# Kernel tuning notes

Measured on AMD Instinct MI355X. Metric: run time of the kernel, lower is better.

Reference implementation:

```python
import jax, jax.numpy as jnp
import numpy as np

B, S, E, H = 4, 2048, 1024, 16
DK = E // H  # 64


def setup_inputs() -> dict:
    key = jax.random.key(0)
    ks = jax.random.split(key, 11)
    s_in = 1.0 / np.sqrt(E)
    return {
        "query": jax.random.normal(ks[0], (B, S, E), jnp.float32),
        "key_": jax.random.normal(ks[1], (B, S, E), jnp.float32),
        "value": jax.random.normal(ks[2], (B, S, E), jnp.float32),
        # nn.Linear weights stored as [out, in]; applied as x @ W.T + b
        "Wq": jax.random.uniform(ks[3], (E, E), jnp.float32, -s_in, s_in),
        "bq": jax.random.uniform(ks[4], (E,), jnp.float32, -s_in, s_in),
        "Wk": jax.random.uniform(ks[5], (E, E), jnp.float32, -s_in, s_in),
        "bk": jax.random.uniform(ks[6], (E,), jnp.float32, -s_in, s_in),
        "Wv": jax.random.uniform(ks[7], (E, E), jnp.float32, -s_in, s_in),
        "bv": jax.random.uniform(ks[8], (E,), jnp.float32, -s_in, s_in),
        "Wo": jax.random.uniform(ks[9], (E, E), jnp.float32, -s_in, s_in),
        "bo": jax.random.uniform(ks[10], (E,), jnp.float32, -s_in, s_in),
    }


def reference(query, key_, value, Wq, bq, Wk, bk, Wv, bv, Wo, bo):
    scale = 1.0 / np.sqrt(DK).astype(np.float32)
    Q = query @ Wq.T + bq   # [B,S,E]
    K = key_ @ Wk.T + bk
    V = value @ Wv.T + bv
    # split heads: [B,S,H,DK] (slicing dim -1 into contiguous per-head chunks)
    Qh = Q.reshape(B, S, H, DK)
    Kh = K.reshape(B, S, H, DK)
    Vh = V.reshape(B, S, H, DK)
    scores = jnp.einsum('bqhd,bkhd->bhqk', Qh, Kh) * scale  # [B,H,S,S]
    probs = jax.nn.softmax(scores, axis=-1)
    ctx = jnp.einsum('bhqk,bkhd->bqhd', probs, Vh).reshape(B, S, E)
    out = ctx @ Wo.T + bo
    return out
```

## Files before the change

kernel.cpp:

```cpp
#include <hip/hip_runtime.h>
#include <stdint.h>
#include <stddef.h>

constexpr int BB = 4, SS = 2048, EE = 1024, HH = 16, DKH = 64;
constexpr int MM = BB * SS;
constexpr float SM_SCALE_LOG2 = 0.18033688011112042f;

typedef unsigned short u16;
typedef __attribute__((ext_vector_type(8))) short bf16x8;
typedef __attribute__((ext_vector_type(8))) unsigned short u16x8;
typedef __attribute__((ext_vector_type(4))) float f32x4;
typedef __attribute__((ext_vector_type(16))) float f32x16;
typedef __attribute__((ext_vector_type(2))) unsigned int u32x2;
typedef __attribute__((ext_vector_type(4))) unsigned int u32x4;

__device__ __forceinline__ u16 f2bf(float f) {
  unsigned u = __builtin_bit_cast(unsigned, f);
  u += 0x7FFFu + ((u >> 16) & 1u);
  return (u16)(u >> 16);
}

__device__ __forceinline__ unsigned pack2(float lo, float hi) {
  unsigned r;
  asm("v_cvt_pk_bf16_f32 %0, %1, %2" : "=v"(r) : "v"(lo), "v"(hi));
  return r;
}

__device__ __forceinline__ void gld16(const void* g, void* l) {
  __builtin_amdgcn_global_load_lds(
      (const __attribute__((address_space(1))) unsigned int*)g,
      (__attribute__((address_space(3))) unsigned int*)l, 16, 0, 0);
}

struct Cvt3 { const float* in[3]; u16* out[3]; };
struct Cvt4 { const float* in[4]; u16* out[4]; };

__global__ void cvt_bf16_x3(Cvt3 p, int n8) {
  int i = blockIdx.x * 256 + threadIdx.x;
  if (i >= n8) return;
  const int z = blockIdx.y;
  const float4* src = (const float4*)p.in[z] + (size_t)i * 2;
  float4 a = src[0], b = src[1];
  u16x8 v;
  v[0] = f2bf(a.x); v[1] = f2bf(a.y); v[2] = f2bf(a.z); v[3] = f2bf(a.w);
  v[4] = f2bf(b.x); v[5] = f2bf(b.y); v[6] = f2bf(b.z); v[7] = f2bf(b.w);
  *((u16x8*)p.out[z] + i) = v;
}

__global__ void cvt_bf16_x4(Cvt4 p, int n8) {
  int i = blockIdx.x * 256 + threadIdx.x;
  if (i >= n8) return;
  const int z = blockIdx.y;
  const float4* src = (const float4*)p.in[z] + (size_t)i * 2;
  float4 a = src[0], b = src[1];
  u16x8 v;
  v[0] = f2bf(a.x); v[1] = f2bf(a.y); v[2] = f2bf(a.z); v[3] = f2bf(a.w);
  v[4] = f2bf(b.x); v[5] = f2bf(b.y); v[6] = f2bf(b.z); v[7] = f2bf(b.w);
  *((u16x8*)p.out[z] + i) = v;
}

struct GemmPtrs {
  const u16* A[3];
  const u16* W[3];
  const float* bias[3];
  void* C[3];
  float scale[3];
  int mode[3];
};

__global__ __launch_bounds__(256, 4) void gemm32(GemmPtrs p, int M, int N, int K) {
  __shared__ __align__(16) u16 SA[2][64 * 64];
  __shared__ __align__(16) u16 SB[2][64 * 64];
  const int t = threadIdx.x, l = t & 63, w = t >> 6;
  const int lq = l & 31, hi = l >> 5;
  const int wm = w >> 1, wn = w & 1;
  const int z = blockIdx.z;
  const u16* A = p.A[z];
  const u16* W = p.W[z];
  const float* bias = p.bias[z];

  const int nwg = gridDim.x * gridDim.y;
  const int o = blockIdx.y * gridDim.x + blockIdx.x;
  const int sw = (o & 7) * (nwg >> 3) + (o >> 3);
  const int n0 = (sw % gridDim.x) * 128;
  const int m0 = (sw / gridDim.x) * 128;

  f32x16 acc[2][2];
#pragma unroll
  for (int i = 0; i < 2; ++i)
#pragma unroll
    for (int j = 0; j < 2; ++j)
#pragma unroll
      for (int r = 0; r < 16; ++r) acc[i][j][r] = 0.f;

  auto stage = [&](int buf, int kt) {
#pragma unroll
    for (int i = 0; i < 2; ++i) {
      const int ci = i * 256 + t;
      const int r = ci >> 3, P = ci & 7;
      const int L = P ^ (r & 7);
      const int m = r + ((L & 4) << 4);
      const int kc = L & 3;
      const int dst = (i * 256 + (t & ~63)) * 16;
      gld16(A + (size_t)(m0 + m) * K + kt * 32 + kc * 8, (char*)&SA[buf][0] + dst);
      gld16(W + (size_t)(n0 + m) * K + kt * 32 + kc * 8, (char*)&SB[buf][0] + dst);
    }
  };

  stage(0, 0);
  __syncthreads();
  int cur = 0;
  const int NT = K >> 5;
  const int lsw = lq & 7;
  for (int kt = 0; kt < NT; ++kt) {
    if (kt + 1 < NT) stage(cur ^ 1, kt + 1);
    const u16* Ac = &SA[cur][0];
    const u16* Bc = &SB[cur][0];
    __builtin_amdgcn_s_setprio(1);
#pragma unroll
    for (int ks = 0; ks < 2; ++ks) {
      const int ca = ((wm << 2) + (ks << 1) + hi) ^ lsw;
      const int cb = ((wn << 2) + (ks << 1) + hi) ^ lsw;
      bf16x8 a0 = *(const bf16x8*)(Ac + lq * 64 + ca * 8);
      bf16x8 a1 = *(const bf16x8*)(Ac + (32 + lq) * 64 + ca * 8);
      bf16x8 b0 = *(const bf16x8*)(Bc + lq * 64 + cb * 8);
      bf16x8 b1 = *(const bf16x8*)(Bc + (32 + lq) * 64 + cb * 8);
      acc[0][0] = __builtin_amdgcn_mfma_f32_32x32x16_bf16(a0, b0, acc[0][0], 0, 0, 0);
      acc[0][1] = __builtin_amdgcn_mfma_f32_32x32x16_bf16(a0, b1, acc[0][1], 0, 0, 0);
      acc[1][0] = __builtin_amdgcn_mfma_f32_32x32x16_bf16(a1, b0, acc[1][0], 0, 0, 0);
      acc[1][1] = __builtin_amdgcn_mfma_f32_32x32x16_bf16(a1, b1, acc[1][1], 0, 0, 0);
    }
    __builtin_amdgcn_s_setprio(0);
    __syncthreads();
    cur ^= 1;
  }

  const float sc = p.scale[z];
  const int mode = p.mode[z];
#pragma unroll
  for (int fr = 0; fr < 2; ++fr) {
#pragma unroll
    for (int fc = 0; fc < 2; ++fc) {
      const int col = n0 + wn * 64 + fc * 32 + lq;
      const float bv = bias[col];
#pragma unroll
      for (int g = 0; g < 4; ++g) {
        const int mb = m0 + wm * 64 + fr * 32 + 8 * g + 4 * hi;
        float v[4];
#pragma unroll
        for (int j = 0; j < 4; ++j) v[j] = (acc[fr][fc][4 * g + j] + bv) * sc;
        if (mode == 1) {
#pragma unroll
          for (int j = 0; j < 4; ++j)
            ((float*)p.C[z])[(size_t)(mb + j) * N + col] = v[j];
        } else if (mode == 0) {
#pragma unroll
          for (int j = 0; j < 4; ++j)
            ((u16*)p.C[z])[(size_t)(mb + j) * N + col] = f2bf(v[j]);
        } else {
          const int b = mb >> 11, s = mb & 2047;
          u16* dst = (u16*)p.C[z] +
                     ((size_t)((b * 16 + (col >> 6)) * 64 + (col & 63))) * SS + s;
          uint2 pk;
          pk.x = pack2(v[0], v[1]);
          pk.y = pack2(v[2], v[3]);
          *(uint2*)dst = pk;
        }
      }
    }
  }
}

__global__ __launch_bounds__(256, 4) void attn_fwd3(const u16* __restrict__ Q,
                                                    const u16* __restrict__ K,
                                                    const u16* __restrict__ Vt,
                                                    u16* __restrict__ C) {
  __shared__ __align__(16) u16 Ks[2][64 * 64];
  __shared__ __align__(16) u16 Vs[2][64 * 64];

  const int t = threadIdx.x, l = t & 63, w = t >> 6;
  const int lq = l & 31, hi = l >> 5;
  const int q0 = blockIdx.x * 128;
  const int bh = blockIdx.y, bb = bh >> 4, hh = bh & 15;

  const u16* qp = Q + ((size_t)(bb * SS + q0 + w * 32 + lq)) * EE + hh * 64 + hi * 8;
  bf16x8 qf[4];
  qf[0] = *(const bf16x8*)(qp);
  qf[1] = *(const bf16x8*)(qp + 16);
  qf[2] = *(const bf16x8*)(qp + 32);
  qf[3] = *(const bf16x8*)(qp + 48);

  const u16* Kbase = K + (size_t)bb * SS * EE + hh * 64;
  const u16* Vbase = Vt + (size_t)bh * DKH * SS;

  f32x16 accA, accB;
  f32x16 z16;
#pragma unroll
  for (int i = 0; i < 16; ++i) { accA[i] = 0.f; accB[i] = 0.f; z16[i] = 0.f; }
  float lsum = 0.0f;

  auto stage = [&](int buf, int kt) {
#pragma unroll
    for (int i = 0; i < 2; ++i) {
      const int slot = i * 256 + t;
      const int row = slot >> 3, pc = slot & 7;
      const int lc = pc ^ (row & 7);
      const int lbyte = (i * 256 + (t & ~63)) * 16;
      gld16(Kbase + (size_t)(kt * 64 + row) * EE + lc * 8, (char*)&Ks[buf][0] + lbyte);
      gld16(Vbase + (size_t)row * SS + kt * 64 + lc * 8, (char*)&Vs[buf][0] + lbyte);
    }
  };

  auto mkfrag = [&](const f32x16& p, int base) -> bf16x8 {
    unsigned A0 = pack2(p[base + 0], p[base + 1]);
    unsigned A1 = pack2(p[base + 2], p[base + 3]);
    unsigned B0 = pack2(p[base + 4], p[base + 5]);
    unsigned B1 = pack2(p[base + 6], p[base + 7]);
    u32x2 r0 = __builtin_amdgcn_permlane32_swap(A0, B0, false, false);
    u32x2 r1 = __builtin_amdgcn_permlane32_swap(A1, B1, false, false);
    u32x4 fr;
    fr[0] = r0[0]; fr[1] = r1[0]; fr[2] = r0[1]; fr[3] = r1[1];
    return __builtin_bit_cast(bf16x8, fr);
  };

  stage(0, 0);
  __syncthreads();
  int cur = 0;
  for (int kt = 0; kt < SS / 64; ++kt) {
    if (kt + 1 < SS / 64) stage(cur ^ 1, kt + 1);
    const u16* Kc = &Ks[cur][0];
    const u16* Vc = &Vs[cur][0];

    f32x16 s0, s1;
    __builtin_amdgcn_s_setprio(1);
    {
      const int c = hi ^ (lq & 7);
      bf16x8 kf0 = *(const bf16x8*)(Kc + lq * 64 + c * 8);
      bf16x8 kf1 = *(const bf16x8*)(Kc + (32 + lq) * 64 + c * 8);
      s0 = __builtin_amdgcn_mfma_f32_32x32x16_bf16(kf0, qf[0], z16, 0, 0, 0);
      s1 = __builtin_amdgcn_mfma_f32_32x32x16_bf16(kf1, qf[0], z16, 0, 0, 0);
    }
#pragma unroll
    for (int m = 1; m < 4; ++m) {
      const int c = (2 * m + hi) ^ (lq & 7);
      bf16x8 kf0 = *(const bf16x8*)(Kc + lq * 64 + c * 8);
      bf16x8 kf1 = *(const bf16x8*)(Kc + (32 + lq) * 64 + c * 8);
      s0 = __builtin_amdgcn_mfma_f32_32x32x16_bf16(kf0, qf[m], s0, 0, 0, 0);
      s1 = __builtin_amdgcn_mfma_f32_32x32x16_bf16(kf1, qf[m], s1, 0, 0, 0);
    }
    __builtin_amdgcn_s_setprio(0);

#pragma unroll
    for (int i = 0; i < 16; ++i) {
      s0[i] = __builtin_amdgcn_exp2f(s0[i]);
      s1[i] = __builtin_amdgcn_exp2f(s1[i]);
    }
    float sa = 0.f, sb = 0.f, sc2 = 0.f, sd = 0.f;
#pragma unroll
    for (int i = 0; i < 8; ++i) {
      sa += s0[i]; sb += s0[i + 8];
      sc2 += s1[i]; sd += s1[i + 8];
    }
    lsum += (sa + sb) + (sc2 + sd);

    bf16x8 pf[4];
    pf[0] = mkfrag(s0, 0);
    pf[1] = mkfrag(s0, 8);
    pf[2] = mkfrag(s1, 0);
    pf[3] = mkfrag(s1, 8);

    __builtin_amdgcn_s_setprio(1);
#pragma unroll
    for (int s = 0; s < 4; ++s) {
      const int c = (2 * s + hi) ^ (lq & 7);
      bf16x8 vf0 = *(const bf16x8*)(Vc + lq * 64 + c * 8);
      bf16x8 vf1 = *(const bf16x8*)(Vc + (32 + lq) * 64 + c * 8);
      accA = __builtin_amdgcn_mfma_f32_32x32x16_bf16(vf0, pf[s], accA, 0, 0, 0);
      accB = __builtin_amdgcn_mfma_f32_32x32x16_bf16(vf1, pf[s], accB, 0, 0, 0);
    }
    __builtin_amdgcn_s_setprio(0);
    __syncthreads();
    cur ^= 1;
  }

  const float inv = 1.0f / (lsum + __shfl_xor(lsum, 32));
  char* Tw = (char*)&Ks[0][0] + w * 4096;
#pragma unroll
  for (int g = 0; g < 4; ++g) {
    uint2 pa, pb;
    pa.x = pack2(accA[4 * g + 0] * inv, accA[4 * g + 1] * inv);
    pa.y = pack2(accA[4 * g + 2] * inv, accA[4 * g + 3] * inv);
    pb.x = pack2(accB[4 * g + 0] * inv, accB[4 * g + 1] * inv);
    pb.y = pack2(accB[4 * g + 2] * inv, accB[4 * g + 3] * inv);
    const int sub = 8 * hi, sw = (lq & 7) << 4;
    *(uint2*)(Tw + lq * 128 + (((g) << 4) ^ sw) + sub) = pa;
    *(uint2*)(Tw + lq * 128 + (((4 + g) << 4) ^ sw) + sub) = pb;
  }
  const int qr0 = l >> 3, ch = l & 7;
#pragma unroll
  for (int ps = 0; ps < 4; ++ps) {
    const int qr = ps * 8 + qr0;
    u32x4 vv = *(const u32x4*)(Tw + qr * 128 + ((ch ^ (qr & 7)) << 4));
    u16* dst = C + ((size_t)(bb * SS + q0 + w * 32 + qr)) * EE + hh * 64 + ch * 8;
    *(u32x4*)dst = vv;
  }
}

extern "C" void kernel_launch(void* const* d_in, const int* in_sizes, int n_in,
                              void* d_out, int out_size, void* d_ws, size_t ws_size,
                              hipStream_t stream) {
  (void)in_sizes; (void)n_in; (void)out_size; (void)ws_size;
  const float* query = (const float*)d_in[0];
  const float* key_  = (const float*)d_in[1];
  const float* value = (const float*)d_in[2];
  const float* Wq = (const float*)d_in[3];
  const float* bq = (const float*)d_in[4];
  const float* Wk = (const float*)d_in[5];
  const float* bk = (const float*)d_in[6];
  const float* Wv = (const float*)d_in[7];
  const float* bv = (const float*)d_in[8];
  const float* Wo = (const float*)d_in[9];
  const float* bo = (const float*)d_in[10];

  char* ws = (char*)d_ws;
  const size_t SZX = (size_t)MM * EE * 2;
  const size_t SZW = (size_t)EE * EE * 2;
  u16* Xq  = (u16*)(ws + 0 * SZX);
  u16* Xk  = (u16*)(ws + 1 * SZX);
  u16* Xv  = (u16*)(ws + 2 * SZX);
  u16* Qb  = (u16*)(ws + 3 * SZX);
  u16* Kb  = (u16*)(ws + 4 * SZX);
  u16* Vtb = (u16*)(ws + 5 * SZX);
  u16* Cb  = (u16*)(ws + 6 * SZX);
  u16* Wqb = (u16*)(ws + 7 * SZX + 0 * SZW);
  u16* Wkb = (u16*)(ws + 7 * SZX + 1 * SZW);
  u16* Wvb = (u16*)(ws + 7 * SZX + 2 * SZW);
  u16* Wob = (u16*)(ws + 7 * SZX + 3 * SZW);

  const int n8x = MM * EE / 8;
  const int n8w = EE * EE / 8;

  Cvt3 cx{};
  cx.in[0] = query; cx.in[1] = key_; cx.in[2] = value;
  cx.out[0] = Xq; cx.out[1] = Xk; cx.out[2] = Xv;
  cvt_bf16_x3<<<dim3(n8x / 256, 3), 256, 0, stream>>>(cx, n8x);

  Cvt4 cw{};
  cw.in[0] = Wq; cw.in[1] = Wk; cw.in[2] = Wv; cw.in[3] = Wo;
  cw.out[0] = Wqb; cw.out[1] = Wkb; cw.out[2] = Wvb; cw.out[3] = Wob;
  cvt_bf16_x4<<<dim3(n8w / 256, 4), 256, 0, stream>>>(cw, n8w);

  GemmPtrs g{};
  g.A[0] = Xq; g.A[1] = Xk; g.A[2] = Xv;
  g.W[0] = Wqb; g.W[1] = Wkb; g.W[2] = Wvb;
  g.bias[0] = bq; g.bias[1] = bk; g.bias[2] = bv;
  g.C[0] = Qb; g.C[1] = Kb; g.C[2] = Vtb;
  g.scale[0] = SM_SCALE_LOG2; g.scale[1] = 1.0f; g.scale[2] = 1.0f;
  g.mode[0] = 0; g.mode[1] = 0; g.mode[2] = 2;
  gemm32<<<dim3(EE / 128, MM / 128, 3), 256, 0, stream>>>(g, MM, EE, EE);

  attn_fwd3<<<dim3(SS / 128, BB * HH), 256, 0, stream>>>(Qb, Kb, Vtb, Cb);

  GemmPtrs g2{};
  g2.A[0] = Cb; g2.W[0] = Wob; g2.bias[0] = bo; g2.C[0] = d_out;
  g2.scale[0] = 1.0f; g2.mode[0] = 1;
  gemm32<<<dim3(EE / 128, MM / 128, 1), 256, 0, stream>>>(g2, MM, EE, EE);
}
```

Baseline: 211.8 us.

## Fuse fp32-to-bf16 activation conversion into QKV projection GEMM A-tile staging

New measurement: 217.4 us. 2.7% more time.

```diff
diff --git a/kernel.cpp b/kernel.cpp
--- a/kernel.cpp
+++ b/kernel.cpp
@@ -32,20 +32,7 @@
       (__attribute__((address_space(3))) unsigned int*)l, 16, 0, 0);
 }
 
-struct Cvt3 { const float* in[3]; u16* out[3]; };
 struct Cvt4 { const float* in[4]; u16* out[4]; };
-
-__global__ void cvt_bf16_x3(Cvt3 p, int n8) {
-  int i = blockIdx.x * 256 + threadIdx.x;
-  if (i >= n8) return;
-  const int z = blockIdx.y;
-  const float4* src = (const float4*)p.in[z] + (size_t)i * 2;
-  float4 a = src[0], b = src[1];
-  u16x8 v;
-  v[0] = f2bf(a.x); v[1] = f2bf(a.y); v[2] = f2bf(a.z); v[3] = f2bf(a.w);
-  v[4] = f2bf(b.x); v[5] = f2bf(b.y); v[6] = f2bf(b.z); v[7] = f2bf(b.w);
-  *((u16x8*)p.out[z] + i) = v;
-}
 
 __global__ void cvt_bf16_x4(Cvt4 p, int n8) {
   int i = blockIdx.x * 256 + threadIdx.x;
@@ -61,6 +48,7 @@
 
 struct GemmPtrs {
   const u16* A[3];
+  const float* A32[3];
   const u16* W[3];
   const float* bias[3];
   void* C[3];
@@ -68,6 +56,7 @@
   int mode[3];
 };
 
+template <int AF32>
 __global__ __launch_bounds__(256, 4) void gemm32(GemmPtrs p, int M, int N, int K) {
   __shared__ __align__(16) u16 SA[2][64 * 64];
   __shared__ __align__(16) u16 SB[2][64 * 64];
@@ -76,6 +65,7 @@
   const int wm = w >> 1, wn = w & 1;
   const int z = blockIdx.z;
   const u16* A = p.A[z];
+  const float* Af = p.A32[z];
   const u16* W = p.W[z];
   const float* bias = p.bias[z];
 
@@ -93,27 +83,76 @@
 #pragma unroll
       for (int r = 0; r < 16; ++r) acc[i][j][r] = 0.f;
 
-  auto stage = [&](int buf, int kt) {
+  auto stageB = [&](int buf, int kt) {
 #pragma unroll
     for (int i = 0; i < 2; ++i) {
       const int ci = i * 256 + t;
       const int r = ci >> 3, P = ci & 7;
       const int L = P ^ (r & 7);
-      const int m = r + ((L & 4) << 4);
+      const int mr = r + ((L & 4) << 4);
       const int kc = L & 3;
-      const int dst = (i * 256 + (t & ~63)) * 16;
-      gld16(A + (size_t)(m0 + m) * K + kt * 32 + kc * 8, (char*)&SA[buf][0] + dst);
-      gld16(W + (size_t)(n0 + m) * K + kt * 32 + kc * 8, (char*)&SB[buf][0] + dst);
-    }
-  };
-
-  stage(0, 0);
+      gld16(W + (size_t)(n0 + mr) * K + kt * 32 + kc * 8,
+            (char*)&SB[buf][0] + (i * 256 + (t & ~63)) * 16);
+    }
+  };
+  auto stageAb = [&](int buf, int kt) {
+#pragma unroll
+    for (int i = 0; i < 2; ++i) {
+      const int ci = i * 256 + t;
+      const int r = ci >> 3, P = ci & 7;
+      const int L = P ^ (r & 7);
+      const int mr = r + ((L & 4) << 4);
+      const int kc = L & 3;
+      gld16(A + (size_t)(m0 + mr) * K + kt * 32 + kc * 8,
+            (char*)&SA[buf][0] + (i * 256 + (t & ~63)) * 16);
+    }
+  };
+  float4 av[2][2];
+  auto loadAf = [&](int kt) {
+#pragma unroll
+    for (int i = 0; i < 2; ++i) {
+      const int u = i * 256 + t;
+      const int mr = u >> 2, kc = u & 3;
+      const float4* src = (const float4*)(Af + (size_t)(m0 + mr) * K + kt * 32 + kc * 8);
+      av[i][0] = src[0];
+      av[i][1] = src[1];
+    }
+  };
+  auto writeAf = [&](int buf) {
+#pragma unroll
+    for (int i = 0; i < 2; ++i) {
+      const int u = i * 256 + t;
+      const int mr = u >> 2, kc = u & 3;
+      const int r = mr & 63;
+      const int P = (((mr >> 6) << 2) + kc) ^ (r & 7);
+      u32x4 pk;
+      pk[0] = pack2(av[i][0].x, av[i][0].y);
+      pk[1] = pack2(av[i][0].z, av[i][0].w);
+      pk[2] = pack2(av[i][1].x, av[i][1].y);
+      pk[3] = pack2(av[i][1].z, av[i][1].w);
+      *(u32x4*)((char*)&SA[buf][0] + r * 128 + P * 16) = pk;
+    }
+  };
+
+  if (AF32) {
+    loadAf(0);
+    writeAf(0);
+  } else {
+    stageAb(0, 0);
+  }
+  stageB(0, 0);
   __syncthreads();
+
   int cur = 0;
   const int NT = K >> 5;
   const int lsw = lq & 7;
   for (int kt = 0; kt < NT; ++kt) {
-    if (kt + 1 < NT) stage(cur ^ 1, kt + 1);
+    const bool nx = (kt + 1 < NT);
+    if (nx) {
+      if (AF32) loadAf(kt + 1);
+      else stageAb(cur ^ 1, kt + 1);
+      stageB(cur ^ 1, kt + 1);
+    }
     const u16* Ac = &SA[cur][0];
     const u16* Bc = &SB[cur][0];
     __builtin_amdgcn_s_setprio(1);
@@ -131,6 +170,10 @@
       acc[1][1] = __builtin_amdgcn_mfma_f32_32x32x16_bf16(a1, b1, acc[1][1], 0, 0, 0);
     }
     __builtin_amdgcn_s_setprio(0);
+    if (AF32 && nx) {
+      __builtin_amdgcn_sched_barrier(0);
+      writeAf(cur ^ 1);
+    }
     __syncthreads();
     cur ^= 1;
   }
@@ -325,25 +368,16 @@
   char* ws = (char*)d_ws;
   const size_t SZX = (size_t)MM * EE * 2;
   const size_t SZW = (size_t)EE * EE * 2;
-  u16* Xq  = (u16*)(ws + 0 * SZX);
-  u16* Xk  = (u16*)(ws + 1 * SZX);
-  u16* Xv  = (u16*)(ws + 2 * SZX);
-  u16* Qb  = (u16*)(ws + 3 * SZX);
-  u16* Kb  = (u16*)(ws + 4 * SZX);
-  u16* Vtb = (u16*)(ws + 5 * SZX);
-  u16* Cb  = (u16*)(ws + 6 * SZX);
-  u16* Wqb = (u16*)(ws + 7 * SZX + 0 * SZW);
-  u16* Wkb = (u16*)(ws + 7 * SZX + 1 * SZW);
-  u16* Wvb = (u16*)(ws + 7 * SZX + 2 * SZW);
-  u16* Wob = (u16*)(ws + 7 * SZX + 3 * SZW);
-
-  const int n8x = MM * EE / 8;
+  u16* Qb  = (u16*)(ws + 0 * SZX);
+  u16* Kb  = (u16*)(ws + 1 * SZX);
+  u16* Vtb = (u16*)(ws + 2 * SZX);
+  u16* Cb  = (u16*)(ws + 3 * SZX);
+  u16* Wqb = (u16*)(ws + 4 * SZX + 0 * SZW);
+  u16* Wkb = (u16*)(ws + 4 * SZX + 1 * SZW);
+  u16* Wvb = (u16*)(ws + 4 * SZX + 2 * SZW);
+  u16* Wob = (u16*)(ws + 4 * SZX + 3 * SZW);
+
   const int n8w = EE * EE / 8;
-
-  Cvt3 cx{};
-  cx.in[0] = query; cx.in[1] = key_; cx.in[2] = value;
-  cx.out[0] = Xq; cx.out[1] = Xk; cx.out[2] = Xv;
-  cvt_bf16_x3<<<dim3(n8x / 256, 3), 256, 0, stream>>>(cx, n8x);
 
   Cvt4 cw{};
   cw.in[0] = Wq; cw.in[1] = Wk; cw.in[2] = Wv; cw.in[3] = Wo;
@@ -351,18 +385,18 @@
   cvt_bf16_x4<<<dim3(n8w / 256, 4), 256, 0, stream>>>(cw, n8w);
 
   GemmPtrs g{};
-  g.A[0] = Xq; g.A[1] = Xk; g.A[2] = Xv;
+  g.A32[0] = query; g.A32[1] = key_; g.A32[2] = value;
   g.W[0] = Wqb; g.W[1] = Wkb; g.W[2] = Wvb;
   g.bias[0] = bq; g.bias[1] = bk; g.bias[2] = bv;
   g.C[0] = Qb; g.C[1] = Kb; g.C[2] = Vtb;
   g.scale[0] = SM_SCALE_LOG2; g.scale[1] = 1.0f; g.scale[2] = 1.0f;
   g.mode[0] = 0; g.mode[1] = 0; g.mode[2] = 2;
-  gemm32<<<dim3(EE / 128, MM / 128, 3), 256, 0, stream>>>(g, MM, EE, EE);
+  gemm32<1><<<dim3(EE / 128, MM / 128, 3), 256, 0, stream>>>(g, MM, EE, EE);
 
   attn_fwd3<<<dim3(SS / 128, BB * HH), 256, 0, stream>>>(Qb, Kb, Vtb, Cb);
 
   GemmPtrs g2{};
   g2.A[0] = Cb; g2.W[0] = Wob; g2.bias[0] = bo; g2.C[0] = d_out;
   g2.scale[0] = 1.0f; g2.mode[0] = 1;
-  gemm32<<<dim3(EE / 128, MM / 128, 1), 256, 0, stream>>>(g2, MM, EE, EE);
-}
+  gemm32<0><<<dim3(EE / 128, MM / 128, 1), 256, 0, stream>>>(g2, MM, EE, EE);
+}
```

## Triple-buffer GEMM LDS stages with manual vmcnt waits and single barrier

Applied to the files above, without the earlier changes.

Result: slower. 217.2 us (+2.6%).

```diff
diff --git a/kernel.cpp b/kernel.cpp
--- a/kernel.cpp
+++ b/kernel.cpp
@@ -69,8 +69,8 @@
 };
 
 __global__ __launch_bounds__(256, 4) void gemm32(GemmPtrs p, int M, int N, int K) {
-  __shared__ __align__(16) u16 SA[2][64 * 64];
-  __shared__ __align__(16) u16 SB[2][64 * 64];
+  __shared__ __align__(16) u16 SA[3][64 * 64];
+  __shared__ __align__(16) u16 SB[3][64 * 64];
   const int t = threadIdx.x, l = t & 63, w = t >> 6;
   const int lq = l & 31, hi = l >> 5;
   const int wm = w >> 1, wn = w & 1;
@@ -107,32 +107,42 @@
     }
   };
 
-  stage(0, 0);
-  __syncthreads();
-  int cur = 0;
   const int NT = K >> 5;
   const int lsw = lq & 7;
+
+  stage(0, 0);
+  stage(1, 1);
   for (int kt = 0; kt < NT; ++kt) {
-    if (kt + 1 < NT) stage(cur ^ 1, kt + 1);
-    const u16* Ac = &SA[cur][0];
-    const u16* Bc = &SB[cur][0];
-    __builtin_amdgcn_s_setprio(1);
+    const int cb = kt % 3;
+    if (kt + 1 < NT)
+      asm volatile("s_waitcnt vmcnt(4)" ::: "memory");
+    else
+      asm volatile("s_waitcnt vmcnt(0)" ::: "memory");
+    asm volatile("s_barrier" ::: "memory");
+    if (kt + 2 < NT) stage((kt + 2) % 3, kt + 2);
+    const u16* Ac = &SA[cb][0];
+    const u16* Bc = &SB[cb][0];
+    bf16x8 a0[2], a1[2], b0[2], b1[2];
 #pragma unroll
     for (int ks = 0; ks < 2; ++ks) {
       const int ca = ((wm << 2) + (ks << 1) + hi) ^ lsw;
-      const int cb = ((wn << 2) + (ks << 1) + hi) ^ lsw;
-      bf16x8 a0 = *(const bf16x8*)(Ac + lq * 64 + ca * 8);
-      bf16x8 a1 = *(const bf16x8*)(Ac + (32 + lq) * 64 + ca * 8);
-      bf16x8 b0 = *(const bf16x8*)(Bc + lq * 64 + cb * 8);
-      bf16x8 b1 = *(const bf16x8*)(Bc + (32 + lq) * 64 + cb * 8);
-      acc[0][0] = __builtin_amdgcn_mfma_f32_32x32x16_bf16(a0, b0, acc[0][0], 0, 0, 0);
-      acc[0][1] = __builtin_amdgcn_mfma_f32_32x32x16_bf16(a0, b1, acc[0][1], 0, 0, 0);
-      acc[1][0] = __builtin_amdgcn_mfma_f32_32x32x16_bf16(a1, b0, acc[1][0], 0, 0, 0);
-      acc[1][1] = __builtin_amdgcn_mfma_f32_32x32x16_bf16(a1, b1, acc[1][1], 0, 0, 0);
+      const int cbk = ((wn << 2) + (ks << 1) + hi) ^ lsw;
+      a0[ks] = *(const bf16x8*)(Ac + lq * 64 + ca * 8);
+      a1[ks] = *(const bf16x8*)(Ac + (32 + lq) * 64 + ca * 8);
+      b0[ks] = *(const bf16x8*)(Bc + lq * 64 + cbk * 8);
+      b1[ks] = *(const bf16x8*)(Bc + (32 + lq) * 64 + cbk * 8);
+    }
+    asm volatile("s_waitcnt lgkmcnt(0)" ::: "memory");
+    __builtin_amdgcn_sched_barrier(0);
+    __builtin_amdgcn_s_setprio(1);
+#pragma unroll
+    for (int ks = 0; ks < 2; ++ks) {
+      acc[0][0] = __builtin_amdgcn_mfma_f32_32x32x16_bf16(a0[ks], b0[ks], acc[0][0], 0, 0, 0);
+      acc[0][1] = __builtin_amdgcn_mfma_f32_32x32x16_bf16(a0[ks], b1[ks], acc[0][1], 0, 0, 0);
+      acc[1][0] = __builtin_amdgcn_mfma_f32_32x32x16_bf16(a1[ks], b0[ks], acc[1][0], 0, 0, 0);
+      acc[1][1] = __builtin_amdgcn_mfma_f32_32x32x16_bf16(a1[ks], b1[ks], acc[1][1], 0, 0, 0);
     }
     __builtin_amdgcn_s_setprio(0);
-    __syncthreads();
-    cur ^= 1;
   }
 
   const float sc = p.scale[z];
```
